# Kernel tuning notes

Hardware: AMD Instinct MI355X
Metric: run time of the kernel (lower is better)

## Reference

```python
import jax, jax.numpy as jnp
import numpy as np

IMAGE_SIZE = 512
MAX_BOXES = 150
SCORE_THRESH = 0.3
IOU_THRESH = 0.1
BATCH = 32
NUM_CLASS = 20


def setup_inputs():
    key = jax.random.key(0)
    k0, k1, k2, k3 = jax.random.split(key, 4)
    ch = 3 * (5 + NUM_CLASS)  # 75
    fm0 = jax.random.normal(k0, (BATCH, 16, 16, ch), jnp.float32)  # stride 32
    fm1 = jax.random.normal(k1, (BATCH, 32, 32, ch), jnp.float32)  # stride 16
    fm2 = jax.random.normal(k2, (BATCH, 64, 64, ch), jnp.float32)  # stride 8
    # 9 (w,h) anchor sizes in pixels, sorted small->large like YOLOv3
    anchors = jnp.sort(jax.random.uniform(k3, (9, 2), jnp.float32, 10.0, 380.0), axis=0)
    return {"fm0": fm0, "fm1": fm1, "fm2": fm2, "anchors": anchors, "CLASS": NUM_CLASS}


def decode_layer(fm, anchors_layer, num_class):
    # fm: [B, gh, gw, 3*(5+C)]; anchors_layer: [3,2] (w,h)
    b, gh, gw, _ = fm.shape
    ratio = jnp.array([IMAGE_SIZE / gh, IMAGE_SIZE / gw], jnp.float32)  # (ry, rx)
    rescaled = anchors_layer / ratio[::-1]  # (w/rx, h/ry)
    fm = fm.reshape(b, gh, gw, 3, 5 + num_class)
    centers = jax.nn.sigmoid(fm[..., :2])
    sizes = fm[..., 2:4]
    conf = fm[..., 4:5]
    prob = fm[..., 5:]
    gx, gy = jnp.meshgrid(jnp.arange(gw), jnp.arange(gh))  # 'xy' indexing, like tf
    offs = jnp.stack([gx, gy], axis=-1).astype(jnp.float32)[None, :, :, None, :]
    centers = (centers + offs) * ratio[::-1]            # to pixel coords
    sizes = jnp.exp(sizes) * rescaled * ratio[::-1]     # to pixel sizes
    N = gh * gw * 3
    boxes = jnp.concatenate([centers, sizes], axis=-1).reshape(b, N, 4)
    return (boxes,
            jax.nn.sigmoid(conf).reshape(b, N, 1),
            jax.nn.sigmoid(prob).reshape(b, N, num_class))


def nms_single(boxes, scores):
    # boxes [N,4] xyxy, scores [N]; returns kept anchor indices [MAX_BOXES] (-1 = empty)
    N = boxes.shape[0]
    neg = jnp.float32(-1e30)
    s = jnp.where(scores > SCORE_THRESH, scores, neg)  # strict > (K.greater)
    order = jnp.argsort(-s)
    sb = boxes[order]
    ss = s[order]
    area = (sb[:, 2] - sb[:, 0]) * (sb[:, 3] - sb[:, 1])

    def body(i, state):
        suppressed, kept = state
        avail = (~suppressed) & (ss > neg)
        pick = jnp.argmax(avail)          # first available in score order
        ok = avail[pick]
        box = sb[pick]
        ix1 = jnp.maximum(box[0], sb[:, 0])
        iy1 = jnp.maximum(box[1], sb[:, 1])
        ix2 = jnp.minimum(box[2], sb[:, 2])
        iy2 = jnp.minimum(box[3], sb[:, 3])
        inter = jnp.maximum(ix2 - ix1, 0.0) * jnp.maximum(iy2 - iy1, 0.0)
        iou = inter / (area[pick] + area - inter)
        suppressed = suppressed | (ok & (iou > IOU_THRESH))  # self-suppresses (iou=1)
        kept = kept.at[i].set(jnp.where(ok, order[pick], -1))
        return suppressed, kept

    init = (jnp.zeros((N,), bool), jnp.full((MAX_BOXES,), -1, jnp.int32))
    _, kept = jax.lax.fori_loop(0, MAX_BOXES, body, init)
    return kept


def nms_image(boxes, cls_scores):
    # boxes [N,4], cls_scores [N,C]
    C = cls_scores.shape[1]
    kept = jax.vmap(nms_single, in_axes=(None, 1))(
        jax.lax.stop_gradient(boxes), jax.lax.stop_gradient(cls_scores))  # [C,150]
    labels = jnp.broadcast_to(jnp.arange(C)[:, None], kept.shape)
    flat_idx = kept.reshape(-1)
    flat_lab = labels.reshape(-1)
    valid = flat_idx >= 0
    safe_idx = jnp.where(valid, flat_idx, 0)
    flat_sc = jnp.where(valid, cls_scores[safe_idx, flat_lab], -1.0)
    top_sc, top_i = jax.lax.top_k(flat_sc, MAX_BOXES)  # global top-k across classes
    sel_idx = flat_idx[top_i]
    sel_lab = flat_lab[top_i]
    sel_ok = top_sc > 0.0  # real scores are > SCORE_THRESH > 0; pads are -1
    out_boxes = jnp.where(sel_ok[:, None], boxes[jnp.where(sel_ok, sel_idx, 0)], -1.0)
    out_scores = jnp.where(sel_ok, top_sc, -1.0)
    out_labels = jnp.where(sel_ok, sel_lab, -1).astype(jnp.int32)
    return out_boxes, out_scores, out_labels


def reference(fm0, fm1, fm2, anchors, CLASS):
    layers = [(fm0, anchors[6:9]), (fm1, anchors[3:6]), (fm2, anchors[0:3])]
    bl, cl, pl = [], [], []
    for fm, anc in layers:
        b, c, p = decode_layer(fm, anc, CLASS)
        bl.append(b); cl.append(c); pl.append(p)
    boxes = jnp.concatenate(bl, axis=1)   # [B,N,4] (cx,cy,w,h)
    conf = jnp.concatenate(cl, axis=1)    # [B,N,1]
    prob = jnp.concatenate(pl, axis=1)    # [B,N,C]
    cx, cy, w, h = boxes[..., 0], boxes[..., 1], boxes[..., 2], boxes[..., 3]
    boxes = jnp.stack([cx - w / 2, cy - h / 2, cx + w / 2, cy + h / 2], axis=-1)
    scores = conf * prob                  # [B,N,C]
    return jax.vmap(nms_image)(boxes, scores)
```

## Files before the change

kernel.cpp:

```cpp
#include <hip/hip_runtime.h>

#define BATCH 32
#define NUM_CLASS 20
#define NTOT 16128
#define N0 768
#define N1 3072
#define MAX_BOXES 150
#define SORT_N 8192
#define CAND_CAP 7600
#define TOPK_N 4096
#define SCORE_THRESH 0.3f
#define IOU_THRESH 0.1f
#define NMS_W 1024
#define TOPK_W 1024

typedef unsigned long long u64;

__device__ __forceinline__ float exp_f32cr(float x) { return (float)exp((double)x); }
__device__ __forceinline__ float sigm(float x) { return 1.0f / (1.0f + exp_f32cr(-x)); }

__device__ __forceinline__ bool iou_rej(float4 kb, float4 c4, float carea) {
    float ix1 = fmaxf(kb.x, c4.x), iy1 = fmaxf(kb.y, c4.y);
    float ix2 = fminf(kb.z, c4.z), iy2 = fminf(kb.w, c4.w);
    float inter = fmaxf(ix2 - ix1, 0.0f) * fmaxf(iy2 - iy1, 0.0f);
    float ka = (kb.z - kb.x) * (kb.w - kb.y);
    return (inter / (ka + carea - inter)) > IOU_THRESH;
}

template<int VPT>
__device__ __forceinline__ void bitonic_reg_sort(u64* lds, int tid, int nthreads) {
    const int N = nthreads * VPT;
    u64 r[VPT];
    #pragma unroll
    for (int e = 0; e < VPT; ++e) r[e] = lds[tid * VPT + e];

    for (int k = 2; k <= N; k <<= 1) {
        int j = k >> 1;
        for (; j >= 64 * VPT; j >>= 1) {
            __syncthreads();
            #pragma unroll
            for (int e = 0; e < VPT; ++e) lds[tid * VPT + e] = r[e];
            __syncthreads();
            #pragma unroll
            for (int e = 0; e < VPT; ++e) {
                int i = tid * VPT + e;
                u64 q = lds[i ^ j];
                bool takeMin = (((i & k) == 0) == ((i & j) == 0));
                bool less = r[e] < q;
                r[e] = (takeMin == less) ? r[e] : q;
            }
        }
        for (; j >= VPT; j >>= 1) {
            int ld = j / VPT;
            #pragma unroll
            for (int e = 0; e < VPT; ++e) {
                unsigned lo = (unsigned)r[e], hi = (unsigned)(r[e] >> 32);
                lo = (unsigned)__shfl_xor((int)lo, ld);
                hi = (unsigned)__shfl_xor((int)hi, ld);
                u64 q = ((u64)hi << 32) | lo;
                int i = tid * VPT + e;
                bool takeMin = (((i & k) == 0) == ((i & j) == 0));
                bool less = r[e] < q;
                r[e] = (takeMin == less) ? r[e] : q;
            }
        }
        for (; j >= 1; j >>= 1) {
            #pragma unroll
            for (int e = 0; e < VPT; ++e) {
                int p = e ^ j;
                if (p > e) {
                    int i = tid * VPT + e;
                    bool up = ((i & k) == 0);
                    u64 a = r[e], bkey = r[p];
                    if (up ? (a > bkey) : (a < bkey)) { r[e] = bkey; r[p] = a; }
                }
            }
        }
    }
    __syncthreads();
    #pragma unroll
    for (int e = 0; e < VPT; ++e) lds[tid * VPT + e] = r[e];
    __syncthreads();
}

__global__ __launch_bounds__(256) void decode_kernel(
    const float* __restrict__ fm0, const float* __restrict__ fm1,
    const float* __restrict__ fm2, const float* __restrict__ anchors,
    float* __restrict__ boxes, float* __restrict__ scores)
{
    int t = blockIdx.x * 256 + threadIdx.x;
    if (t >= BATCH * NTOT) return;
    int b = t / NTOT, n = t % NTOT;
    const float* fm; int g, arow, local;
    if (n < N0)           { fm = fm0; g = 16; arow = 6; local = n; }
    else if (n < N0 + N1) { fm = fm1; g = 32; arow = 3; local = n - N0; }
    else                  { fm = fm2; g = 64; arow = 0; local = n - (N0 + N1); }
    int cell = local / 3, a = local % 3;
    int gy = cell / g, gx = cell % g;
    const float* p = fm + ((size_t)((b * g + gy) * g + gx) * 75 + (size_t)a * 25);
    float s = 512.0f / (float)g;
    float cx = (sigm(p[0]) + (float)gx) * s;
    float cy = (sigm(p[1]) + (float)gy) * s;
    float w = exp_f32cr(p[2]) * anchors[(arow + a) * 2 + 0];
    float h = exp_f32cr(p[3]) * anchors[(arow + a) * 2 + 1];
    float conf = sigm(p[4]);
    float* bo = boxes + (size_t)t * 4;
    bo[0] = cx - w * 0.5f;
    bo[1] = cy - h * 0.5f;
    bo[2] = cx + w * 0.5f;
    bo[3] = cy + h * 0.5f;
    size_t sb = (size_t)b * NUM_CLASS * NTOT + (size_t)n;
    #pragma unroll
    for (int c = 0; c < NUM_CLASS; ++c)
        scores[sb + (size_t)c * NTOT] = conf * sigm(p[5 + c]);
}

__global__ __launch_bounds__(NMS_W) void sort_kernel(
    const float* __restrict__ scores, u64* __restrict__ skeys,
    int* __restrict__ scnt_g)
{
    __shared__ u64 keys[SORT_N];
    __shared__ unsigned scnt_s;

    const int tid = threadIdx.x;
    const int wlane = tid & 63;
    const int bc = blockIdx.x;

    if (tid == 0) scnt_s = 0u;
    __syncthreads();

    const float* sc = scores + (size_t)bc * NTOT;
    for (int n0 = 0; n0 < NTOT; n0 += NMS_W) {
        int n = n0 + tid;
        float s = (n < NTOT) ? sc[n] : -1.0f;
        bool pass = s > SCORE_THRESH;
        u64 m = __ballot(pass);
        unsigned base = 0;
        if (wlane == 0 && m) base = atomicAdd(&scnt_s, (unsigned)__popcll(m));
        base = __shfl(base, 0);
        if (pass) {
            unsigned pos = base + (unsigned)__popcll(m & ((1ull << wlane) - 1ull));
            if (pos < CAND_CAP) {
                unsigned sbits = ~__float_as_uint(s);
                keys[pos] = ((u64)sbits << 32) | (unsigned)n;
            }
        }
    }
    __syncthreads();
    int cnt = (int)scnt_s; if (cnt > CAND_CAP) cnt = CAND_CAP;
    for (int i = cnt + tid; i < SORT_N; i += NMS_W) keys[i] = ~0ull;
    __syncthreads();

    bitonic_reg_sort<SORT_N / NMS_W>(keys, tid, NMS_W);

    u64* ko = skeys + (size_t)bc * SORT_N;
    #pragma unroll
    for (int r = 0; r < SORT_N / NMS_W; ++r)
        ko[r * NMS_W + tid] = keys[r * NMS_W + tid];
    if (tid == 0) scnt_g[bc] = cnt;
}

__global__ __launch_bounds__(64) void scan_kernel(
    const float* __restrict__ boxes, const u64* __restrict__ skeys,
    const int* __restrict__ scnt_g,
    int* __restrict__ kept_idx, float* __restrict__ kept_score)
{
    __shared__ float4 kept[MAX_BOXES + 4];
    const int lane = threadIdx.x;
    const int bc = blockIdx.x;
    const int b  = bc / NUM_CLASS;

    for (int i = lane; i < MAX_BOXES + 4; i += 64)
        kept[i] = make_float4(1e30f, 1e30f, 1e30f, 1e30f);
    __syncthreads();

    const u64* keys = skeys + (size_t)bc * SORT_N;
    int cnt = scnt_g[bc]; if (cnt > CAND_CAP) cnt = CAND_CAP;
    const float* bbase = boxes + (size_t)b * NTOT * 4;
    const size_t obase = (size_t)bc * MAX_BOXES;
    int nk = 0;

    for (int s0 = 0; s0 < cnt && nk < MAX_BOXES; s0 += 64) {
        int i = s0 + lane;
        int state = 1;
        float4 c4 = make_float4(0.f, 0.f, 0.f, 0.f);
        float cs = 0.0f, carea = 0.0f; int cn = -1;
        if (i < cnt) {
            u64 key = keys[i];
            cn = (int)(key & 0xffffffffull);
            cs = __uint_as_float(~(unsigned)(key >> 32));
            c4 = *(const float4*)(bbase + (size_t)cn * 4);
            carea = (c4.z - c4.x) * (c4.w - c4.y);
            state = 0;
            int nk4 = (nk + 3) & ~3;
            for (int kk = 0; kk < nk4; kk += 4) {
                float4 k0 = kept[kk], k1 = kept[kk + 1];
                float4 k2 = kept[kk + 2], k3 = kept[kk + 3];
                bool rej = iou_rej(k0, c4, carea) | iou_rej(k1, c4, carea)
                         | iou_rej(k2, c4, carea) | iou_rej(k3, c4, carea);
                if (rej) { state = 1; break; }
            }
        }
        while (nk < MAX_BOXES) {
            u64 m = __ballot(state == 0);
            if (!m) break;
            int fi = (int)__builtin_ctzll(m);
            float4 kb;
            kb.x = __shfl(c4.x, fi); kb.y = __shfl(c4.y, fi);
            kb.z = __shfl(c4.z, fi); kb.w = __shfl(c4.w, fi);
            int   kn = __shfl(cn, fi);
            float ks = __shfl(cs, fi);
            if (lane == 0) {
                kept[nk] = kb;
                kept_idx  [obase + nk] = kn;
                kept_score[obase + nk] = ks;
            }
            if (lane == fi) state = 2;
            else if (state == 0 && iou_rej(kb, c4, carea)) state = 1;
            ++nk;
        }
        __syncthreads();
    }
    for (int kx = nk + lane; kx < MAX_BOXES; kx += 64) {
        kept_idx  [obase + kx] = -1;
        kept_score[obase + kx] = -1.0f;
    }
}

__global__ __launch_bounds__(TOPK_W) void topk_kernel(
    const float* __restrict__ boxes, const int* __restrict__ kept_idx,
    const float* __restrict__ kept_score, float* __restrict__ out)
{
    __shared__ u64 keys[TOPK_N];
    const int tid = threadIdx.x;
    const int b = blockIdx.x;
    const int FLAT = NUM_CLASS * MAX_BOXES;

    for (int f = tid; f < TOPK_N; f += TOPK_W) {
        u64 key = ~0ull;
        if (f < FLAT) {
            int idx = kept_idx[(size_t)b * FLAT + f];
            float s = (idx >= 0) ? kept_score[(size_t)b * FLAT + f] : -1.0f;
            unsigned u = __float_as_uint(s);
            unsigned mm = (u & 0x80000000u) ? ~u : (u | 0x80000000u);
            key = ((u64)(~mm) << 32) | (unsigned)f;
        }
        keys[f] = key;
    }
    __syncthreads();

    bitonic_reg_sort<TOPK_N / TOPK_W>(keys, tid, TOPK_W);

    if (tid < MAX_BOXES) {
        u64 key = keys[tid];
        int f = (int)(key & 0xffffffffull);
        float sc = -1.0f; int idx = -1;
        if (f < FLAT) {
            idx = kept_idx[(size_t)b * FLAT + f];
            if (idx >= 0) sc = kept_score[(size_t)b * FLAT + f];
        }
        bool ok = (idx >= 0) && (sc > 0.0f);
        float bx0 = -1.0f, bx1 = -1.0f, bx2 = -1.0f, bx3 = -1.0f;
        float lab = -1.0f;
        if (ok) {
            const float* bp = boxes + ((size_t)b * NTOT + idx) * 4;
            bx0 = bp[0]; bx1 = bp[1]; bx2 = bp[2]; bx3 = bp[3];
            lab = (float)(f / MAX_BOXES);
        } else {
            sc = -1.0f;
        }
        float* ob = out + ((size_t)b * MAX_BOXES + tid) * 4;
        ob[0] = bx0; ob[1] = bx1; ob[2] = bx2; ob[3] = bx3;
        out[(size_t)BATCH * MAX_BOXES * 4 + (size_t)b * MAX_BOXES + tid] = sc;
        out[(size_t)BATCH * MAX_BOXES * 5 + (size_t)b * MAX_BOXES + tid] = lab;
    }
}

extern "C" void kernel_launch(void* const* d_in, const int* in_sizes, int n_in,
                              void* d_out, int out_size, void* d_ws, size_t ws_size,
                              hipStream_t stream) {
    const float* fm0 = (const float*)d_in[0];
    const float* fm1 = (const float*)d_in[1];
    const float* fm2 = (const float*)d_in[2];
    const float* anchors = (const float*)d_in[3];
    float* out = (float*)d_out;

    float* boxes  = (float*)d_ws;
    float* scores = boxes + (size_t)BATCH * NTOT * 4;
    u64*   skeys  = (u64*)(scores + (size_t)BATCH * NUM_CLASS * NTOT);
    int*   scnt   = (int*)(skeys + (size_t)BATCH * NUM_CLASS * SORT_N);
    int*   kept_idx   = scnt + BATCH * NUM_CLASS;
    float* kept_score = (float*)(kept_idx + (size_t)BATCH * NUM_CLASS * MAX_BOXES);

    int total = BATCH * NTOT;
    decode_kernel<<<(total + 255) / 256, 256, 0, stream>>>(fm0, fm1, fm2, anchors, boxes, scores);
    sort_kernel<<<BATCH * NUM_CLASS, NMS_W, 0, stream>>>(scores, skeys, scnt);
    scan_kernel<<<BATCH * NUM_CLASS, 64, 0, stream>>>(boxes, skeys, scnt, kept_idx, kept_score);
    topk_kernel<<<BATCH, TOPK_W, 0, stream>>>(boxes, kept_idx, kept_score, out);
}
```

Measured before the change: 455.8 us.

## Swizzle LDS sort layout, write sorted keys from registers, prefetch NMS candidates

Applies an XOR swizzle to LDS indices in the bitonic sort so strided per-thread accesses avoid bank conflicts. The sort kernel now writes sorted keys straight from registers to global memory, skipping the final LDS store and its barriers. The scan kernel prefetches the next chunk of 64 candidate keys and boxes while the current chunk is processed, caches kept-box areas in shared memory, and unrolls the IoU check over 8 kept boxes. The prefetch reads keys past cnt, which stays within the padded SORT_N buffer.

```diff
diff --git a/kernel.cpp b/kernel.cpp
--- a/kernel.cpp
+++ b/kernel.cpp
@@ -19,32 +19,32 @@
 __device__ __forceinline__ float exp_f32cr(float x) { return (float)exp((double)x); }
 __device__ __forceinline__ float sigm(float x) { return 1.0f / (1.0f + exp_f32cr(-x)); }
 
-__device__ __forceinline__ bool iou_rej(float4 kb, float4 c4, float carea) {
+__device__ __forceinline__ bool iou_rej2(float4 kb, float ka, float4 c4, float carea) {
     float ix1 = fmaxf(kb.x, c4.x), iy1 = fmaxf(kb.y, c4.y);
     float ix2 = fminf(kb.z, c4.z), iy2 = fminf(kb.w, c4.w);
     float inter = fmaxf(ix2 - ix1, 0.0f) * fmaxf(iy2 - iy1, 0.0f);
-    float ka = (kb.z - kb.x) * (kb.w - kb.y);
     return (inter / (ka + carea - inter)) > IOU_THRESH;
 }
 
+__device__ __forceinline__ int phys_idx(int i) { return i ^ ((i >> 4) & 0xF); }
+
 template<int VPT>
-__device__ __forceinline__ void bitonic_reg_sort(u64* lds, int tid, int nthreads) {
+__device__ __forceinline__ void bitonic_reg_core(u64 (&r)[VPT], u64* lds, int tid, int nthreads) {
     const int N = nthreads * VPT;
-    u64 r[VPT];
     #pragma unroll
-    for (int e = 0; e < VPT; ++e) r[e] = lds[tid * VPT + e];
+    for (int e = 0; e < VPT; ++e) r[e] = lds[phys_idx(tid * VPT + e)];
 
     for (int k = 2; k <= N; k <<= 1) {
         int j = k >> 1;
         for (; j >= 64 * VPT; j >>= 1) {
             __syncthreads();
             #pragma unroll
-            for (int e = 0; e < VPT; ++e) lds[tid * VPT + e] = r[e];
+            for (int e = 0; e < VPT; ++e) lds[phys_idx(tid * VPT + e)] = r[e];
             __syncthreads();
             #pragma unroll
             for (int e = 0; e < VPT; ++e) {
                 int i = tid * VPT + e;
-                u64 q = lds[i ^ j];
+                u64 q = lds[phys_idx(i ^ j)];
                 bool takeMin = (((i & k) == 0) == ((i & j) == 0));
                 bool less = r[e] < q;
                 r[e] = (takeMin == less) ? r[e] : q;
@@ -77,10 +77,6 @@
             }
         }
     }
-    __syncthreads();
-    #pragma unroll
-    for (int e = 0; e < VPT; ++e) lds[tid * VPT + e] = r[e];
-    __syncthreads();
 }
 
 __global__ __launch_bounds__(256) void decode_kernel(
@@ -142,21 +138,22 @@
             unsigned pos = base + (unsigned)__popcll(m & ((1ull << wlane) - 1ull));
             if (pos < CAND_CAP) {
                 unsigned sbits = ~__float_as_uint(s);
-                keys[pos] = ((u64)sbits << 32) | (unsigned)n;
+                keys[phys_idx((int)pos)] = ((u64)sbits << 32) | (unsigned)n;
             }
         }
     }
     __syncthreads();
     int cnt = (int)scnt_s; if (cnt > CAND_CAP) cnt = CAND_CAP;
-    for (int i = cnt + tid; i < SORT_N; i += NMS_W) keys[i] = ~0ull;
-    __syncthreads();
-
-    bitonic_reg_sort<SORT_N / NMS_W>(keys, tid, NMS_W);
+    for (int i = cnt + tid; i < SORT_N; i += NMS_W) keys[phys_idx(i)] = ~0ull;
+    __syncthreads();
+
+    u64 r[SORT_N / NMS_W];
+    bitonic_reg_core<SORT_N / NMS_W>(r, keys, tid, NMS_W);
 
     u64* ko = skeys + (size_t)bc * SORT_N;
     #pragma unroll
-    for (int r = 0; r < SORT_N / NMS_W; ++r)
-        ko[r * NMS_W + tid] = keys[r * NMS_W + tid];
+    for (int e = 0; e < SORT_N / NMS_W; ++e)
+        ko[tid * (SORT_N / NMS_W) + e] = r[e];
     if (tid == 0) scnt_g[bc] = cnt;
 }
 
@@ -165,13 +162,16 @@
     const int* __restrict__ scnt_g,
     int* __restrict__ kept_idx, float* __restrict__ kept_score)
 {
-    __shared__ float4 kept[MAX_BOXES + 4];
+    __shared__ float4 kept[MAX_BOXES + 8];
+    __shared__ float  karea_s[MAX_BOXES + 8];
     const int lane = threadIdx.x;
     const int bc = blockIdx.x;
     const int b  = bc / NUM_CLASS;
 
-    for (int i = lane; i < MAX_BOXES + 4; i += 64)
+    for (int i = lane; i < MAX_BOXES + 8; i += 64) {
         kept[i] = make_float4(1e30f, 1e30f, 1e30f, 1e30f);
+        karea_s[i] = 0.0f;
+    }
     __syncthreads();
 
     const u64* keys = skeys + (size_t)bc * SORT_N;
@@ -180,24 +180,30 @@
     const size_t obase = (size_t)bc * MAX_BOXES;
     int nk = 0;
 
+    u64 key_cur = keys[lane];
+    int  cn_cur = (int)(key_cur & 0xffffffffull);
+    bool lv_cur = (lane < cnt);
+    float4 c4_cur = lv_cur ? *(const float4*)(bbase + (size_t)cn_cur * 4)
+                           : make_float4(0.f, 0.f, 0.f, 0.f);
+
     for (int s0 = 0; s0 < cnt && nk < MAX_BOXES; s0 += 64) {
-        int i = s0 + lane;
+        u64 key_nxt = keys[s0 + 64 + lane];
+        int  cn_nxt = (int)(key_nxt & 0xffffffffull);
+        bool lv_nxt = (s0 + 64 + lane) < cnt;
+        float4 c4_nxt = lv_nxt ? *(const float4*)(bbase + (size_t)cn_nxt * 4)
+                               : make_float4(0.f, 0.f, 0.f, 0.f);
+
         int state = 1;
-        float4 c4 = make_float4(0.f, 0.f, 0.f, 0.f);
-        float cs = 0.0f, carea = 0.0f; int cn = -1;
-        if (i < cnt) {
-            u64 key = keys[i];
-            cn = (int)(key & 0xffffffffull);
-            cs = __uint_as_float(~(unsigned)(key >> 32));
-            c4 = *(const float4*)(bbase + (size_t)cn * 4);
-            carea = (c4.z - c4.x) * (c4.w - c4.y);
+        float cs = __uint_as_float(~(unsigned)(key_cur >> 32));
+        float carea = (c4_cur.z - c4_cur.x) * (c4_cur.w - c4_cur.y);
+        if (lv_cur) {
             state = 0;
-            int nk4 = (nk + 3) & ~3;
-            for (int kk = 0; kk < nk4; kk += 4) {
-                float4 k0 = kept[kk], k1 = kept[kk + 1];
-                float4 k2 = kept[kk + 2], k3 = kept[kk + 3];
-                bool rej = iou_rej(k0, c4, carea) | iou_rej(k1, c4, carea)
-                         | iou_rej(k2, c4, carea) | iou_rej(k3, c4, carea);
+            int nk8 = (nk + 7) & ~7;
+            for (int kk = 0; kk < nk8; kk += 8) {
+                bool rej = false;
+                #pragma unroll
+                for (int u = 0; u < 8; ++u)
+                    rej |= iou_rej2(kept[kk + u], karea_s[kk + u], c4_cur, carea);
                 if (rej) { state = 1; break; }
             }
         }
@@ -206,19 +212,22 @@
             if (!m) break;
             int fi = (int)__builtin_ctzll(m);
             float4 kb;
-            kb.x = __shfl(c4.x, fi); kb.y = __shfl(c4.y, fi);
-            kb.z = __shfl(c4.z, fi); kb.w = __shfl(c4.w, fi);
-            int   kn = __shfl(cn, fi);
+            kb.x = __shfl(c4_cur.x, fi); kb.y = __shfl(c4_cur.y, fi);
+            kb.z = __shfl(c4_cur.z, fi); kb.w = __shfl(c4_cur.w, fi);
+            int   kn = __shfl(cn_cur, fi);
             float ks = __shfl(cs, fi);
+            float ka = __shfl(carea, fi);
             if (lane == 0) {
                 kept[nk] = kb;
+                karea_s[nk] = ka;
                 kept_idx  [obase + nk] = kn;
                 kept_score[obase + nk] = ks;
             }
             if (lane == fi) state = 2;
-            else if (state == 0 && iou_rej(kb, c4, carea)) state = 1;
+            else if (state == 0 && iou_rej2(kb, ka, c4_cur, carea)) state = 1;
             ++nk;
         }
+        key_cur = key_nxt; cn_cur = cn_nxt; lv_cur = lv_nxt; c4_cur = c4_nxt;
         __syncthreads();
     }
     for (int kx = nk + lane; kx < MAX_BOXES; kx += 64) {
@@ -245,14 +254,21 @@
             unsigned mm = (u & 0x80000000u) ? ~u : (u | 0x80000000u);
             key = ((u64)(~mm) << 32) | (unsigned)f;
         }
-        keys[f] = key;
-    }
-    __syncthreads();
-
-    bitonic_reg_sort<TOPK_N / TOPK_W>(keys, tid, TOPK_W);
+        keys[phys_idx(f)] = key;
+    }
+    __syncthreads();
+
+    u64 r[TOPK_N / TOPK_W];
+    bitonic_reg_core<TOPK_N / TOPK_W>(r, keys, tid, TOPK_W);
+
+    __syncthreads();
+    #pragma unroll
+    for (int e = 0; e < TOPK_N / TOPK_W; ++e)
+        keys[phys_idx(tid * (TOPK_N / TOPK_W) + e)] = r[e];
+    __syncthreads();
 
     if (tid < MAX_BOXES) {
-        u64 key = keys[tid];
+        u64 key = keys[phys_idx(tid)];
         int f = (int)(key & 0xffffffffull);
         float sc = -1.0f; int idx = -1;
         if (f < FLAT) {
```

After: 419.5 us. 8.0% less time.
